# Performance work log

Hardware: AMD Instinct MI355X
Metric: run time of the kernel (lower is better)

The kernel has to match this reference:

```python
import jax, jax.numpy as jnp
import numpy as np

N, E, F, U, H = 10000, 160000, 128, 128, 8
BN_EPS = 1e-3  # keras BatchNormalization default


def _batch_norm(x, gamma, beta):
    # GraphBatchNormalization in training mode: stats over the flat node/edge axis
    mean = jnp.mean(x, axis=0, keepdims=True)
    var = jnp.var(x, axis=0, keepdims=True)
    return (x - mean) * jax.lax.rsqrt(var + BN_EPS) * gamma + beta


def setup_inputs() -> dict:
    key = jax.random.key(0)
    k = jax.random.split(key, 12)
    s = 0.1  # weight init scale
    return {
        "node_attributes": jax.random.normal(k[0], (N, F), jnp.float32),
        "edge_attributes": jax.random.normal(k[1], (E, F), jnp.float32),
        "edge_indices": jax.random.randint(k[2], (E, 2), 0, N, jnp.int32),
        "W_edge": jax.random.normal(k[3], (3 * F, U), jnp.float32) * s,
        "b_edge": jnp.zeros((U,), jnp.float32),
        "gamma_e": jnp.ones((U,), jnp.float32),
        "beta_e": jnp.zeros((U,), jnp.float32),
        "W_node": jax.random.normal(k[4], (F, U), jnp.float32) * s,
        "b_node": jnp.zeros((U,), jnp.float32),
        "gamma_n": jnp.ones((U,), jnp.float32),
        "beta_n": jnp.zeros((U,), jnp.float32),
        "W_att": jax.random.normal(k[5], (H, F, U), jnp.float32) * s,
        "b_att": jnp.zeros((H, U), jnp.float32),
        "a_att": jax.random.normal(k[6], (H, 3 * U), jnp.float32) * s,
        "gru_kernel": jax.random.normal(k[7], (U, 3 * U), jnp.float32) * s,
        "gru_rkernel": jax.random.normal(k[8], (U, 3 * U), jnp.float32) * s,
        "gru_bias": jnp.zeros((2, 3 * U), jnp.float32),
    }


def reference(node_attributes, edge_attributes, edge_indices, W_edge, b_edge,
              gamma_e, beta_e, W_node, b_node, gamma_n, beta_n,
              W_att, b_att, a_att, gru_kernel, gru_rkernel, gru_bias):
    dst = edge_indices[:, 0]  # receiving (ingoing) node per edge
    src = edge_indices[:, 1]  # sending (outgoing) node per edge

    # gather -> concat -> edge MLP -> graph batch norm
    edge_in = node_attributes[src]   # GatherNodesOutgoing
    edge_out = node_attributes[dst]  # GatherNodesIngoing
    edge_concat = jnp.concatenate([edge_in, edge_out, edge_attributes], axis=-1)  # [E, 3F]
    edge_updated = jax.nn.relu(edge_concat @ W_edge + b_edge)
    edge_updated = _batch_norm(edge_updated, gamma_e, beta_e)  # [E, U]

    # multi-head GAT attention over edges, aggregated to receiving node
    z = jnp.einsum('nf,hfu->hnu', node_attributes, W_att) + b_att[:, None, :]  # [H,N,U]
    a_src, a_dst, a_edge = jnp.split(a_att, 3, axis=-1)  # each [H,U]
    s_src = jnp.einsum('hnu,hu->hn', z, a_src)[:, src]           # [H,E]
    s_dst = jnp.einsum('hnu,hu->hn', z, a_dst)[:, dst]           # [H,E]
    s_edge = jnp.einsum('eu,hu->he', edge_updated, a_edge)       # [H,E]
    logits = jax.nn.leaky_relu(s_src + s_dst + s_edge, 0.2)

    seg_max = jax.vmap(lambda l: jax.ops.segment_max(l, dst, num_segments=N))(logits)  # [H,N]
    ex = jnp.exp(logits - seg_max[:, dst])
    den = jax.vmap(lambda e: jax.ops.segment_sum(e, dst, num_segments=N))(ex)          # [H,N]
    alpha = ex / den[:, dst]                                                            # [H,E]

    msgs = alpha[:, :, None] * z[:, src]  # [H,E,U]
    agg = jax.vmap(lambda m: jax.ops.segment_sum(m, dst, num_segments=N))(msgs)  # [H,N,U]
    node_attended = jax.nn.relu(jnp.mean(agg, axis=0))  # [N,U]

    # node MLP + graph batch norm
    node_updated = jax.nn.relu(node_attributes @ W_node + b_node)
    node_updated = _batch_norm(node_updated, gamma_n, beta_n)  # [N,U]

    # GRU update (keras GRUCell, reset_after=True): input=node_attended, state=node_updated
    mx = node_attended @ gru_kernel + gru_bias[0]
    mi = node_updated @ gru_rkernel + gru_bias[1]
    xz, xr, xh = jnp.split(mx, 3, axis=-1)
    rz, rr, rh = jnp.split(mi, 3, axis=-1)
    zg = jax.nn.sigmoid(xz + rz)
    rg = jax.nn.sigmoid(xr + rr)
    hh = jnp.tanh(xh + rg * rh)
    node_final = zg * node_updated + (1.0 - zg) * hh

    return node_final, edge_updated
```

## Files before the change

### kernel.cpp

```cpp
#include <hip/hip_runtime.h>
#include <hip/hip_bf16.h>

#define NN 10000
#define EE 160000
#define FF 128
#define UU 128
#define HH 8
#define BN_EPS 1e-3f

typedef __attribute__((ext_vector_type(8))) short bf16x8;
typedef __attribute__((ext_vector_type(8))) unsigned short u16x8;
typedef __attribute__((ext_vector_type(4))) unsigned short u16x4;
typedef __attribute__((ext_vector_type(4))) unsigned int u32x4;
typedef __attribute__((ext_vector_type(4))) float f32x4;
typedef __attribute__((ext_vector_type(2))) float f32x2;

static __device__ __forceinline__ unsigned short f2bf(float f) {
    unsigned u = __float_as_uint(f);
    u += 0x7fffu + ((u >> 16) & 1u);
    return (unsigned short)(u >> 16);
}
static __device__ __forceinline__ float bf2f(unsigned short b) {
    return __uint_as_float((unsigned)b << 16);
}

__global__ void k_prep(const float* __restrict__ node, unsigned short* __restrict__ node_bf,
                       const float* __restrict__ We, unsigned short* __restrict__ WtE,
                       const float* __restrict__ Wn, unsigned short* __restrict__ WnT,
                       const float* __restrict__ Watt, unsigned short* __restrict__ WtA,
                       const float* __restrict__ Wk, const float* __restrict__ Wr,
                       unsigned short* __restrict__ WcT) {
    int b = blockIdx.x, t = threadIdx.x;
    if (b < 1250) {
        int i = b * 256 + t;
        float4 v = reinterpret_cast<const float4*>(node)[i];
        ushort4 o;
        o.x = f2bf(v.x); o.y = f2bf(v.y); o.z = f2bf(v.z); o.w = f2bf(v.w);
        reinterpret_cast<ushort4*>(node_bf)[i] = o;
    } else if (b < 1442) {
        int i = (b - 1250) * 256 + t;
        int s = i >> 14, rem = i & 16383, u = rem >> 7, k = rem & 127;
        WtE[i] = f2bf(We[(s * 128 + k) * 128 + u]);
    } else if (b < 1506) {
        int i = (b - 1442) * 256 + t;
        int k = i >> 7, u = i & 127;
        WnT[u * 128 + k] = f2bf(Wn[i]);
    } else if (b < 2018) {
        int i = (b - 1506) * 256 + t;
        int h = i >> 14, rem = i & 16383, f = rem >> 7, u = rem & 127;
        WtA[h * 16384 + u * 128 + f] = f2bf(Watt[i]);
    } else {
        int i = (b - 2018) * 256 + t;
        int c = i >> 8, k = i & 255;
        float v;
        if (c < 256)       v = (k < 128) ? Wk[k * 384 + c] : Wr[(k - 128) * 384 + c];
        else if (c < 384)  v = (k < 128) ? Wk[k * 384 + c] : 0.f;
        else               v = (k < 128) ? 0.f : Wr[(k - 128) * 384 + (c - 128)];
        WcT[c * 256 + k] = f2bf(v);
    }
}

__global__ void k_hist(const int* __restrict__ eidx, int* __restrict__ cnt, int E) {
    int e = blockIdx.x * 256 + threadIdx.x;
    if (e < E) atomicAdd(&cnt[eidx[2 * e]], 1);
}

__global__ void k_scan(const int* __restrict__ cnt, int* __restrict__ off,
                       int* __restrict__ cursor, int N) {
    __shared__ int wpre[16];
    __shared__ int runsh;
    int t = threadIdx.x, lane = t & 63, wv = t >> 6;
    if (t == 0) { off[0] = 0; runsh = 0; }
    __syncthreads();
    for (int base = 0; base < N; base += 1024) {
        int x = (base + t < N) ? cnt[base + t] : 0;
        int s = x;
#pragma unroll
        for (int o = 1; o < 64; o <<= 1) {
            int v = __shfl_up(s, o, 64);
            if (lane >= o) s += v;
        }
        if (lane == 63) wpre[wv] = s;
        __syncthreads();
        if (t == 0) {
            int acc = runsh;
#pragma unroll
            for (int i = 0; i < 16; ++i) { int tmp = wpre[i]; wpre[i] = acc; acc += tmp; }
            runsh = acc;
        }
        __syncthreads();
        int inc = s + wpre[wv];
        if (base + t < N) {
            off[base + t + 1] = inc;
            cursor[base + t] = inc - x;
        }
        __syncthreads();
    }
}

__global__ void k_scatter(const int* __restrict__ eidx, int* __restrict__ cursor,
                          int* __restrict__ elist, int E) {
    int e = blockIdx.x * 256 + threadIdx.x;
    if (e < E) {
        int d = eidx[2 * e];
        int p = atomicAdd(&cursor[d], 1);
        elist[p] = e;
    }
}

__global__ void __launch_bounds__(256) k_z8(
        const unsigned short* __restrict__ node_bf, const unsigned short* __restrict__ WtA,
        const float* __restrict__ batt, const float* __restrict__ aatt,
        unsigned char* __restrict__ zt8, float* __restrict__ s_src, float* __restrict__ s_dst) {
    __shared__ unsigned short lds[16 * 1032];
    int n0 = blockIdx.x * 16;
    int t = threadIdx.x;
    {
        int r = t >> 4, c = t & 15;
        *reinterpret_cast<uint4*>(&lds[r * 136 + c * 8]) =
            *reinterpret_cast<const uint4*>(node_bf + (size_t)(n0 + r) * 128 + c * 8);
    }
    __syncthreads();

    int wid = t >> 6, lane = t & 63;
    int lr = lane & 15, lg = lane >> 4;

    f32x4 acc[2][8];
#pragma unroll
    for (int hh = 0; hh < 2; ++hh)
#pragma unroll
        for (int nt = 0; nt < 8; ++nt) acc[hh][nt] = (f32x4){0.f, 0.f, 0.f, 0.f};

#pragma unroll
    for (int ks = 0; ks < 4; ++ks) {
        int kb = ks * 32 + lg * 8;
        bf16x8 a = *reinterpret_cast<const bf16x8*>(&lds[lr * 136 + kb]);
#pragma unroll
        for (int hh = 0; hh < 2; ++hh) {
            const unsigned short* Wh = WtA + (size_t)(wid * 2 + hh) * 16384;
#pragma unroll
            for (int nt = 0; nt < 8; ++nt) {
                bf16x8 b = *reinterpret_cast<const bf16x8*>(Wh + (size_t)(nt * 16 + lr) * 128 + kb);
                acc[hh][nt] = __builtin_amdgcn_mfma_f32_16x16x32_bf16(a, b, acc[hh][nt], 0, 0, 0);
            }
        }
    }

    __syncthreads();
    int head0 = wid * 2, head1 = wid * 2 + 1;
    float ps[2][4], pd[2][4];
#pragma unroll
    for (int hh = 0; hh < 2; ++hh)
#pragma unroll
        for (int r = 0; r < 4; ++r) { ps[hh][r] = 0.f; pd[hh][r] = 0.f; }

#pragma unroll
    for (int nt = 0; nt < 8; ++nt) {
        int col = nt * 16 + lr;
        float b0 = batt[head0 * 128 + col], b1 = batt[head1 * 128 + col];
        float as0 = aatt[head0 * 384 + col], ad0 = aatt[head0 * 384 + 128 + col];
        float as1 = aatt[head1 * 384 + col], ad1 = aatt[head1 * 384 + 128 + col];
#pragma unroll
        for (int r = 0; r < 4; ++r) {
            int row = lg * 4 + r;
            float z0 = acc[0][nt][r] + b0;
            float z1 = acc[1][nt][r] + b1;
            unsigned pk = __builtin_amdgcn_cvt_pk_fp8_f32(z0, z1, 0, false);
            lds[row * 520 + col * 4 + wid] = (unsigned short)(pk & 0xffffu);
            ps[0][r] = fmaf(z0, as0, ps[0][r]);
            pd[0][r] = fmaf(z0, ad0, pd[0][r]);
            ps[1][r] = fmaf(z1, as1, ps[1][r]);
            pd[1][r] = fmaf(z1, ad1, pd[1][r]);
        }
    }
#pragma unroll
    for (int o = 1; o < 16; o <<= 1) {
#pragma unroll
        for (int hh = 0; hh < 2; ++hh)
#pragma unroll
            for (int r = 0; r < 4; ++r) {
                ps[hh][r] += __shfl_xor(ps[hh][r], o, 64);
                pd[hh][r] += __shfl_xor(pd[hh][r], o, 64);
            }
    }
    if (lr == 0) {
#pragma unroll
        for (int hh = 0; hh < 2; ++hh) {
            int head = wid * 2 + hh;
#pragma unroll
            for (int r = 0; r < 4; ++r) {
                int n = n0 + lg * 4 + r;
                s_src[n * 8 + head] = ps[hh][r];
                s_dst[n * 8 + head] = pd[hh][r];
            }
        }
    }
    __syncthreads();
    unsigned short* zt8u = reinterpret_cast<unsigned short*>(zt8);
    for (int q = t; q < 16 * 64; q += 256) {
        int row = q >> 6, c = q & 63;
        *reinterpret_cast<uint4*>(&zt8u[(size_t)(n0 + row) * 512 + c * 8]) =
            *reinterpret_cast<const uint4*>(&lds[row * 520 + c * 8]);
    }
}

__global__ void k_lsum(const float* __restrict__ s_src, const float* __restrict__ s_edge,
                       const int* __restrict__ elist, const int* __restrict__ eidx,
                       float* __restrict__ ls, int* __restrict__ srcl) {
    int p = blockIdx.x * 256 + threadIdx.x;
    if (p >= EE) return;
    int e = elist[p];
    int src = eidx[2 * e + 1];
    srcl[p] = src;
    float4 a0 = *reinterpret_cast<const float4*>(s_src + (size_t)src * 8);
    float4 a1 = *reinterpret_cast<const float4*>(s_src + (size_t)src * 8 + 4);
    float4 b0 = *reinterpret_cast<const float4*>(s_edge + (size_t)e * 8);
    float4 b1 = *reinterpret_cast<const float4*>(s_edge + (size_t)e * 8 + 4);
    float4 o0, o1;
    o0.x = a0.x + b0.x; o0.y = a0.y + b0.y; o0.z = a0.z + b0.z; o0.w = a0.w + b0.w;
    o1.x = a1.x + b1.x; o1.y = a1.y + b1.y; o1.z = a1.z + b1.z; o1.w = a1.w + b1.w;
    *reinterpret_cast<float4*>(ls + (size_t)p * 8) = o0;
    *reinterpret_cast<float4*>(ls + (size_t)p * 8 + 4) = o1;
}

__global__ void __launch_bounds__(256) k_p12_mfma(
        const unsigned short* __restrict__ node_bf, const unsigned short* __restrict__ WtE,
        unsigned short* __restrict__ p12, int N) {
    __shared__ unsigned short ash[64][136];
    int n0 = blockIdx.x * 64;
    int s = blockIdx.y;
    int t = threadIdx.x;
    for (int q = t; q < 64 * 16; q += 256) {
        int r = q >> 4, c = q & 15;
        int n = n0 + r; if (n >= N) n = N - 1;
        *reinterpret_cast<uint4*>(&ash[r][c * 8]) =
            *reinterpret_cast<const uint4*>(node_bf + (size_t)n * 128 + c * 8);
    }
    __syncthreads();

    int wid = t >> 6, lane = t & 63;
    int wm = wid >> 1, wn = wid & 1;
    int lr = lane & 15, lg = lane >> 4;

    f32x4 acc[2][4];
#pragma unroll
    for (int m = 0; m < 2; ++m)
#pragma unroll
        for (int n = 0; n < 4; ++n) acc[m][n] = (f32x4){0.f, 0.f, 0.f, 0.f};

    const unsigned short* Wh = WtE + (size_t)s * 16384;
#pragma unroll
    for (int ks = 0; ks < 4; ++ks) {
        int kb = ks * 32 + lg * 8;
        bf16x8 a0 = *reinterpret_cast<const bf16x8*>(&ash[wm * 32 + lr][kb]);
        bf16x8 a1 = *reinterpret_cast<const bf16x8*>(&ash[wm * 32 + 16 + lr][kb]);
        bf16x8 b[4];
#pragma unroll
        for (int n = 0; n < 4; ++n)
            b[n] = *reinterpret_cast<const bf16x8*>(Wh + (size_t)(wn * 64 + n * 16 + lr) * 128 + kb);
#pragma unroll
        for (int n = 0; n < 4; ++n) {
            acc[0][n] = __builtin_amdgcn_mfma_f32_16x16x32_bf16(a0, b[n], acc[0][n], 0, 0, 0);
            acc[1][n] = __builtin_amdgcn_mfma_f32_16x16x32_bf16(a1, b[n], acc[1][n], 0, 0, 0);
        }
    }

    __syncthreads();
    unsigned short* ot = &ash[0][0];
#pragma unroll
    for (int n = 0; n < 4; ++n) {
        int col = wn * 64 + n * 16 + lr;
#pragma unroll
        for (int m = 0; m < 2; ++m) {
            int rowb = wm * 32 + m * 16 + lg * 4;
#pragma unroll
            for (int r = 0; r < 4; ++r)
                ot[(rowb + r) * 136 + col] = f2bf(acc[m][n][r]);
        }
    }
    __syncthreads();
    for (int q = t; q < 64 * 16; q += 256) {
        int r = q >> 4, c = q & 15;
        int row = n0 + r;
        if (row < N)
            *reinterpret_cast<uint4*>(&p12[(size_t)row * 256 + s * 128 + c * 8]) =
                *reinterpret_cast<const uint4*>(&ot[r * 136 + c * 8]);
    }
}

__global__ void __launch_bounds__(256) k_pe_comb(
        const float* __restrict__ eattr, const unsigned short* __restrict__ WtE,
        const float* __restrict__ be, const unsigned short* __restrict__ p12,
        const int* __restrict__ eidx, unsigned short* __restrict__ ebuf,
        float* __restrict__ part) {
    __shared__ unsigned short ash[64][136];
    __shared__ unsigned short pcomb[64][136];
    __shared__ int sd[128];
    __shared__ float sbuf[4][64], qbuf[4][64];
    int e0 = blockIdx.x * 64;
    int t = threadIdx.x;
    if (t < 128) sd[t] = eidx[e0 * 2 + t];
    __syncthreads();
    for (int q = t; q < 64 * 32; q += 256) {
        int r = q >> 5, c = q & 31;
        f32x4 v = __builtin_nontemporal_load(
            reinterpret_cast<const f32x4*>(eattr + (size_t)(e0 + r) * 128 + c * 4));
        ushort4 o;
        o.x = f2bf(v.x); o.y = f2bf(v.y); o.z = f2bf(v.z); o.w = f2bf(v.w);
        *reinterpret_cast<ushort4*>(&ash[r][c * 4]) = o;
    }
    for (int q = t; q < 64 * 16; q += 256) {
        int r = q >> 4, c = q & 15;
        int dst = sd[r * 2], src = sd[r * 2 + 1];
        u16x8 a = *reinterpret_cast<const u16x8*>(p12 + (size_t)src * 256 + c * 8);
        u16x8 b = *reinterpret_cast<const u16x8*>(p12 + (size_t)dst * 256 + 128 + c * 8);
        u16x8 o;
#pragma unroll
        for (int j = 0; j < 8; ++j) o[j] = f2bf(bf2f(a[j]) + bf2f(b[j]));
        *reinterpret_cast<u16x8*>(&pcomb[r][c * 8]) = o;
    }
    __syncthreads();

    int wid = t >> 6, lane = t & 63;
    int wm = wid >> 1, wn = wid & 1;
    int lr = lane & 15, lg = lane >> 4;

    f32x4 acc[2][4];
#pragma unroll
    for (int m = 0; m < 2; ++m)
#pragma unroll
        for (int n = 0; n < 4; ++n) acc[m][n] = (f32x4){0.f, 0.f, 0.f, 0.f};

    const unsigned short* Wh = WtE + (size_t)2 * 16384;
#pragma unroll
    for (int ks = 0; ks < 4; ++ks) {
        int kb = ks * 32 + lg * 8;
        bf16x8 a0 = *reinterpret_cast<const bf16x8*>(&ash[wm * 32 + lr][kb]);
        bf16x8 a1 = *reinterpret_cast<const bf16x8*>(&ash[wm * 32 + 16 + lr][kb]);
        bf16x8 b[4];
#pragma unroll
        for (int n = 0; n < 4; ++n)
            b[n] = *reinterpret_cast<const bf16x8*>(Wh + (size_t)(wn * 64 + n * 16 + lr) * 128 + kb);
#pragma unroll
        for (int n = 0; n < 4; ++n) {
            acc[0][n] = __builtin_amdgcn_mfma_f32_16x16x32_bf16(a0, b[n], acc[0][n], 0, 0, 0);
            acc[1][n] = __builtin_amdgcn_mfma_f32_16x16x32_bf16(a1, b[n], acc[1][n], 0, 0, 0);
        }
    }

    __syncthreads();
    unsigned short* ot = &ash[0][0];
    float s[4] = {0.f, 0.f, 0.f, 0.f}, q[4] = {0.f, 0.f, 0.f, 0.f};
#pragma unroll
    for (int n = 0; n < 4; ++n) {
        int col = wn * 64 + n * 16 + lr;
        float bias = be[col];
#pragma unroll
        for (int m = 0; m < 2; ++m) {
            int rowb = wm * 32 + m * 16 + lg * 4;
#pragma unroll
            for (int r = 0; r < 4; ++r) {
                int row = rowb + r;
                float v = acc[m][n][r] + bias + bf2f(pcomb[row][col]);
                v = v > 0.f ? v : 0.f;
                ot[row * 136 + col] = f2bf(v);
                s[n] += v;
                q[n] += v * v;
            }
        }
    }
#pragma unroll
    for (int n = 0; n < 4; ++n) {
        s[n] += __shfl_xor(s[n], 16, 64);
        s[n] += __shfl_xor(s[n], 32, 64);
        q[n] += __shfl_xor(q[n], 16, 64);
        q[n] += __shfl_xor(q[n], 32, 64);
    }
    if (lane < 16) {
#pragma unroll
        for (int n = 0; n < 4; ++n) {
            sbuf[wid][n * 16 + lane] = s[n];
            qbuf[wid][n * 16 + lane] = q[n];
        }
    }
    __syncthreads();
    for (int q2 = t; q2 < 64 * 16; q2 += 256) {
        int r = q2 >> 4, c = q2 & 15;
        *reinterpret_cast<uint4*>(&ebuf[(size_t)(e0 + r) * 128 + c * 8]) =
            *reinterpret_cast<const uint4*>(&ot[r * 136 + c * 8]);
    }
    if (t < 128) {
        int half = t >> 6, c = t & 63;
        part[(size_t)blockIdx.x * 256 + t] = sbuf[half][c] + sbuf[2 + half][c];
        part[(size_t)blockIdx.x * 256 + 128 + t] = qbuf[half][c] + qbuf[2 + half][c];
    }
}

__global__ void __launch_bounds__(256) k_node_mlp_mfma(
        const unsigned short* __restrict__ node_bf, const unsigned short* __restrict__ WnT,
        const float* __restrict__ bn, unsigned short* __restrict__ nupd_bf,
        float* __restrict__ part, int N) {
    __shared__ unsigned short ash[64][136];
    __shared__ float sbuf[4][64], qbuf[4][64];
    int n0 = blockIdx.x * 64;
    int t = threadIdx.x;
    for (int q = t; q < 64 * 16; q += 256) {
        int r = q >> 4, c = q & 15;
        int n = n0 + r; if (n >= N) n = N - 1;
        *reinterpret_cast<uint4*>(&ash[r][c * 8]) =
            *reinterpret_cast<const uint4*>(node_bf + (size_t)n * 128 + c * 8);
    }
    __syncthreads();

    int wid = t >> 6, lane = t & 63;
    int wm = wid >> 1, wn = wid & 1;
    int lr = lane & 15, lg = lane >> 4;

    f32x4 acc[2][4];
#pragma unroll
    for (int m = 0; m < 2; ++m)
#pragma unroll
        for (int n = 0; n < 4; ++n) acc[m][n] = (f32x4){0.f, 0.f, 0.f, 0.f};

#pragma unroll
    for (int ks = 0; ks < 4; ++ks) {
        int kb = ks * 32 + lg * 8;
        bf16x8 a0 = *reinterpret_cast<const bf16x8*>(&ash[wm * 32 + lr][kb]);
        bf16x8 a1 = *reinterpret_cast<const bf16x8*>(&ash[wm * 32 + 16 + lr][kb]);
        bf16x8 b[4];
#pragma unroll
        for (int n = 0; n < 4; ++n)
            b[n] = *reinterpret_cast<const bf16x8*>(WnT + (size_t)(wn * 64 + n * 16 + lr) * 128 + kb);
#pragma unroll
        for (int n = 0; n < 4; ++n) {
            acc[0][n] = __builtin_amdgcn_mfma_f32_16x16x32_bf16(a0, b[n], acc[0][n], 0, 0, 0);
            acc[1][n] = __builtin_amdgcn_mfma_f32_16x16x32_bf16(a1, b[n], acc[1][n], 0, 0, 0);
        }
    }

    __syncthreads();
    unsigned short* ot = &ash[0][0];
    float s[4] = {0.f, 0.f, 0.f, 0.f}, q[4] = {0.f, 0.f, 0.f, 0.f};
#pragma unroll
    for (int n = 0; n < 4; ++n) {
        int col = wn * 64 + n * 16 + lr;
        float bias = bn[col];
#pragma unroll
        for (int m = 0; m < 2; ++m) {
            int rowb = wm * 32 + m * 16 + lg * 4;
#pragma unroll
            for (int r = 0; r < 4; ++r) {
                int row = n0 + rowb + r;
                float v = acc[m][n][r] + bias;
                v = v > 0.f ? v : 0.f;
                ot[(rowb + r) * 136 + col] = f2bf(v);
                if (row < N) { s[n] += v; q[n] += v * v; }
            }
        }
    }
#pragma unroll
    for (int n = 0; n < 4; ++n) {
        s[n] += __shfl_xor(s[n], 16, 64);
        s[n] += __shfl_xor(s[n], 32, 64);
        q[n] += __shfl_xor(q[n], 16, 64);
        q[n] += __shfl_xor(q[n], 32, 64);
    }
    if (lane < 16) {
#pragma unroll
        for (int n = 0; n < 4; ++n) {
            sbuf[wid][n * 16 + lane] = s[n];
            qbuf[wid][n * 16 + lane] = q[n];
        }
    }
    __syncthreads();
    for (int q2 = t; q2 < 64 * 16; q2 += 256) {
        int r = q2 >> 4, c = q2 & 15;
        int row = n0 + r;
        if (row < N)
            *reinterpret_cast<uint4*>(&nupd_bf[(size_t)row * 128 + c * 8]) =
                *reinterpret_cast<const uint4*>(&ot[r * 136 + c * 8]);
    }
    if (t < 128) {
        int half = t >> 6, c = t & 63;
        part[(size_t)blockIdx.x * 256 + t] = sbuf[half][c] + sbuf[2 + half][c];
        part[(size_t)blockIdx.x * 256 + 128 + t] = qbuf[half][c] + qbuf[2 + half][c];
    }
}

__global__ void k_bn_fin(const float* __restrict__ part, int nblk, float invcnt,
                         const float* __restrict__ g, const float* __restrict__ b,
                         float* __restrict__ scale, float* __restrict__ shift) {
    int u = blockIdx.x;
    int t = threadIdx.x;
    float s = 0.f, q = 0.f;
    for (int i = t; i < nblk; i += 256) {
        s += part[(size_t)i * 256 + u];
        q += part[(size_t)i * 256 + 128 + u];
    }
    __shared__ float ls[4], lq[4];
    for (int o = 32; o > 0; o >>= 1) {
        s += __shfl_down(s, o, 64);
        q += __shfl_down(q, o, 64);
    }
    int lane = t & 63, w = t >> 6;
    if (lane == 0) { ls[w] = s; lq[w] = q; }
    __syncthreads();
    if (t == 0) {
        float S = ls[0] + ls[1] + ls[2] + ls[3];
        float Q = lq[0] + lq[1] + lq[2] + lq[3];
        float mean = S * invcnt;
        float var = Q * invcnt - mean * mean;
        float inv = rsqrtf(var + BN_EPS);
        float sc = g[u] * inv;
        scale[u] = sc;
        shift[u] = b[u] - mean * sc;
    }
}

__global__ void __launch_bounds__(256) k_edge_final(
        const unsigned short* __restrict__ ebuf, const float* __restrict__ scale,
        const float* __restrict__ shift, const float* __restrict__ aatt,
        float* __restrict__ eout, float* __restrict__ s_edge) {
    int t = threadIdx.x;
    int w = t >> 6, lane = t & 63;
    int q = lane & 31, half = lane >> 5;
    int e = blockIdx.x * 8 + w * 2 + half;

    float4 sc = *reinterpret_cast<const float4*>(scale + q * 4);
    float4 sh = *reinterpret_cast<const float4*>(shift + q * 4);
    float4 a4[8];
#pragma unroll
    for (int h = 0; h < 8; ++h)
        a4[h] = *reinterpret_cast<const float4*>(aatt + h * 384 + 256 + q * 4);

    ushort4 xb = *reinterpret_cast<const ushort4*>(ebuf + (size_t)e * 128 + q * 4);
    float4 x;
    x.x = bf2f(xb.x) * sc.x + sh.x;
    x.y = bf2f(xb.y) * sc.y + sh.y;
    x.z = bf2f(xb.z) * sc.z + sh.z;
    x.w = bf2f(xb.w) * sc.w + sh.w;
    *reinterpret_cast<float4*>(eout + (size_t)e * 128 + q * 4) = x;

    float v[8];
#pragma unroll
    for (int h = 0; h < 8; ++h)
        v[h] = x.x * a4[h].x + x.y * a4[h].y + x.z * a4[h].z + x.w * a4[h].w;
#pragma unroll
    for (int o = 1; o < 32; o <<= 1) {
#pragma unroll
        for (int h = 0; h < 8; ++h) v[h] += __shfl_xor(v[h], o, 64);
    }
    if (q == 0) {
#pragma unroll
        for (int h = 0; h < 8; ++h) s_edge[e * 8 + h] = v[h];
    }
}

__global__ void __launch_bounds__(256) k_agg(
        const unsigned char* __restrict__ zt8, const float* __restrict__ ls,
        const int* __restrict__ srcl, const float* __restrict__ s_dst,
        const int* __restrict__ off, unsigned short* __restrict__ cat) {
    int wv = threadIdx.x >> 6, lane = threadIdx.x & 63;
    int n = blockIdx.x * 4 + wv;
    __shared__ float wbuf[4][64][8];
    __shared__ int snbuf[4][64];

    int beg = off[n], end = off[n + 1];
    int deg = end - beg;
    if (deg == 0) {
        cat[(size_t)n * 256 + lane] = 0;
        cat[(size_t)n * 256 + 64 + lane] = 0;
        return;
    }

    float sdh[8];
#pragma unroll
    for (int h = 0; h < 8; ++h) sdh[h] = s_dst[n * 8 + h];

    float den[8], a0v[8], a1v[8];
#pragma unroll
    for (int h = 0; h < 8; ++h) { den[h] = 0.f; a0v[h] = 0.f; a1v[h] = 0.f; }

    for (int c0 = 0; c0 < deg; c0 += 64) {
        int cn = min(64, deg - c0);
        if (lane < cn) {
            int p = beg + c0 + lane;
            snbuf[wv][lane] = srcl[p];
            float4 l0 = *reinterpret_cast<const float4*>(ls + (size_t)p * 8);
            float4 l1 = *reinterpret_cast<const float4*>(ls + (size_t)p * 8 + 4);
            float lg[8] = {l0.x, l0.y, l0.z, l0.w, l1.x, l1.y, l1.z, l1.w};
#pragma unroll
            for (int h = 0; h < 8; ++h) {
                float x = lg[h] + sdh[h];
                x = x >= 0.f ? x : 0.2f * x;
                wbuf[wv][lane][h] = __expf(x);
            }
        }
        for (int i = 0; i < cn; ++i) {
            int sn_i = snbuf[wv][i];
            const unsigned char* zr = zt8 + (size_t)sn_i * 1024 + (size_t)lane * 8;
            uint2 zv0 = *reinterpret_cast<const uint2*>(zr);
            uint2 zv1 = *reinterpret_cast<const uint2*>(zr + 512);
            float4 w0 = *reinterpret_cast<const float4*>(&wbuf[wv][i][0]);
            float4 w1 = *reinterpret_cast<const float4*>(&wbuf[wv][i][4]);
            f32x2 q01 = __builtin_amdgcn_cvt_pk_f32_fp8(zv0.x, false);
            f32x2 q23 = __builtin_amdgcn_cvt_pk_f32_fp8(zv0.x, true);
            f32x2 q45 = __builtin_amdgcn_cvt_pk_f32_fp8(zv0.y, false);
            f32x2 q67 = __builtin_amdgcn_cvt_pk_f32_fp8(zv0.y, true);
            f32x2 r01 = __builtin_amdgcn_cvt_pk_f32_fp8(zv1.x, false);
            f32x2 r23 = __builtin_amdgcn_cvt_pk_f32_fp8(zv1.x, true);
            f32x2 r45 = __builtin_amdgcn_cvt_pk_f32_fp8(zv1.y, false);
            f32x2 r67 = __builtin_amdgcn_cvt_pk_f32_fp8(zv1.y, true);
            den[0] += w0.x; a0v[0] = fmaf(w0.x, q01.x, a0v[0]); a1v[0] = fmaf(w0.x, r01.x, a1v[0]);
            den[1] += w0.y; a0v[1] = fmaf(w0.y, q01.y, a0v[1]); a1v[1] = fmaf(w0.y, r01.y, a1v[1]);
            den[2] += w0.z; a0v[2] = fmaf(w0.z, q23.x, a0v[2]); a1v[2] = fmaf(w0.z, r23.x, a1v[2]);
            den[3] += w0.w; a0v[3] = fmaf(w0.w, q23.y, a0v[3]); a1v[3] = fmaf(w0.w, r23.y, a1v[3]);
            den[4] += w1.x; a0v[4] = fmaf(w1.x, q45.x, a0v[4]); a1v[4] = fmaf(w1.x, r45.x, a1v[4]);
            den[5] += w1.y; a0v[5] = fmaf(w1.y, q45.y, a0v[5]); a1v[5] = fmaf(w1.y, r45.y, a1v[5]);
            den[6] += w1.z; a0v[6] = fmaf(w1.z, q67.x, a0v[6]); a1v[6] = fmaf(w1.z, r67.x, a1v[6]);
            den[7] += w1.w; a0v[7] = fmaf(w1.w, q67.y, a0v[7]); a1v[7] = fmaf(w1.w, r67.y, a1v[7]);
        }
    }
    float r0 = 0.f, r1 = 0.f;
#pragma unroll
    for (int h = 0; h < 8; ++h) {
        float inv = 1.f / den[h];
        r0 = fmaf(a0v[h], inv, r0);
        r1 = fmaf(a1v[h], inv, r1);
    }
    cat[(size_t)n * 256 + lane] = f2bf(fmaxf(r0 * 0.125f, 0.f));
    cat[(size_t)n * 256 + 64 + lane] = f2bf(fmaxf(r1 * 0.125f, 0.f));
}

__global__ void k_gru_pre(const unsigned short* __restrict__ nupd_bf, const float* __restrict__ scale,
                          const float* __restrict__ shift, unsigned short* __restrict__ cat,
                          float* __restrict__ ush) {
    int i = blockIdx.x * 256 + threadIdx.x;
    if (i >= NN * 32) return;
    int n = i >> 5, j4 = (i & 31) * 4;
    ushort4 ub_in = *reinterpret_cast<const ushort4*>(nupd_bf + (size_t)n * 128 + j4);
    float4 sc = *reinterpret_cast<const float4*>(scale + j4);
    float4 sh = *reinterpret_cast<const float4*>(shift + j4);
    float4 uv;
    uv.x = bf2f(ub_in.x) * sc.x + sh.x;
    uv.y = bf2f(ub_in.y) * sc.y + sh.y;
    uv.z = bf2f(ub_in.z) * sc.z + sh.z;
    uv.w = bf2f(ub_in.w) * sc.w + sh.w;
    ushort4 ub;
    ub.x = f2bf(uv.x); ub.y = f2bf(uv.y); ub.z = f2bf(uv.z); ub.w = f2bf(uv.w);
    *reinterpret_cast<ushort4*>(cat + (size_t)n * 256 + 128 + j4) = ub;
    *reinterpret_cast<float4*>(ush + (size_t)n * 128 + j4) = uv;
}

__global__ void __launch_bounds__(256) k_gru_mm(
        const unsigned short* __restrict__ cat, const unsigned short* __restrict__ WcT,
        float* __restrict__ S, int N) {
    __shared__ unsigned short ash[64][264];
    int n0 = blockIdx.x * 64;
    int g = blockIdx.y;
    int t = threadIdx.x;
    for (int q = t; q < 64 * 32; q += 256) {
        int r = q >> 5, c = q & 31;
        int n = n0 + r; if (n >= N) n = N - 1;
        *reinterpret_cast<uint4*>(&ash[r][c * 8]) =
            *reinterpret_cast<const uint4*>(cat + (size_t)n * 256 + c * 8);
    }
    __syncthreads();

    int wid = t >> 6, lane = t & 63;
    int wm = wid >> 1, wn = wid & 1;
    int lr = lane & 15, lg = lane >> 4;

    f32x4 acc[2][4];
#pragma unroll
    for (int m = 0; m < 2; ++m)
#pragma unroll
        for (int n = 0; n < 4; ++n) acc[m][n] = (f32x4){0.f, 0.f, 0.f, 0.f};

    const unsigned short* Wg = WcT + (size_t)g * 128 * 256;
#pragma unroll
    for (int ks = 0; ks < 8; ++ks) {
        int kb = ks * 32 + lg * 8;
        bf16x8 a0 = *reinterpret_cast<const bf16x8*>(&ash[wm * 32 + lr][kb]);
        bf16x8 a1 = *reinterpret_cast<const bf16x8*>(&ash[wm * 32 + 16 + lr][kb]);
        bf16x8 b[4];
#pragma unroll
        for (int n = 0; n < 4; ++n)
            b[n] = *reinterpret_cast<const bf16x8*>(Wg + (size_t)(wn * 64 + n * 16 + lr) * 256 + kb);
#pragma unroll
        for (int n = 0; n < 4; ++n) {
            acc[0][n] = __builtin_amdgcn_mfma_f32_16x16x32_bf16(a0, b[n], acc[0][n], 0, 0, 0);
            acc[1][n] = __builtin_amdgcn_mfma_f32_16x16x32_bf16(a1, b[n], acc[1][n], 0, 0, 0);
        }
    }

    __syncthreads();
    float* otf = reinterpret_cast<float*>(&ash[0][0]);
#pragma unroll
    for (int n = 0; n < 4; ++n) {
        int col = wn * 64 + n * 16 + lr;
#pragma unroll
        for (int m = 0; m < 2; ++m) {
            int rowb = wm * 32 + m * 16 + lg * 4;
#pragma unroll
            for (int r = 0; r < 4; ++r)
                otf[(rowb + r) * 132 + col] = acc[m][n][r];
        }
    }
    __syncthreads();
    for (int q = t; q < 64 * 32; q += 256) {
        int r = q >> 5, c = q & 31;
        int row = n0 + r;
        if (row < N)
            *reinterpret_cast<float4*>(&S[(size_t)row * 512 + g * 128 + c * 4]) =
                *reinterpret_cast<const float4*>(&otf[r * 132 + c * 4]);
    }
}

__global__ void __launch_bounds__(256) k_gru_gates(
        const float* __restrict__ S, const float* __restrict__ ush,
        const float* __restrict__ gbias, float* __restrict__ outp) {
    int t = threadIdx.x;
    int n = blockIdx.x * 2 + (t >> 7);
    int u = t & 127;
    const float* b0 = gbias;
    const float* b1 = gbias + 384;
    float s0 = S[(size_t)n * 512 + u];
    float s1 = S[(size_t)n * 512 + 128 + u];
    float xh = S[(size_t)n * 512 + 256 + u];
    float rh = S[(size_t)n * 512 + 384 + u];
    float zg = 1.f / (1.f + __expf(-(s0 + b0[u] + b1[u])));
    float rg = 1.f / (1.f + __expf(-(s1 + b0[128 + u] + b1[128 + u])));
    float hh = tanhf(xh + b0[256 + u] + rg * (rh + b1[256 + u]));
    float uv = ush[(size_t)n * 128 + u];
    outp[(size_t)n * 128 + u] = zg * uv + (1.f - zg) * hh;
}

extern "C" void kernel_launch(void* const* d_in, const int* in_sizes, int n_in,
                              void* d_out, int out_size, void* d_ws, size_t ws_size,
                              hipStream_t stream) {
    const float* node    = (const float*)d_in[0];
    const float* eattr   = (const float*)d_in[1];
    const int*   eidx    = (const int*)d_in[2];
    const float* We      = (const float*)d_in[3];
    const float* be      = (const float*)d_in[4];
    const float* gamma_e = (const float*)d_in[5];
    const float* beta_e  = (const float*)d_in[6];
    const float* Wn      = (const float*)d_in[7];
    const float* bnb     = (const float*)d_in[8];
    const float* gamma_n = (const float*)d_in[9];
    const float* beta_n  = (const float*)d_in[10];
    const float* Watt    = (const float*)d_in[11];
    const float* batt    = (const float*)d_in[12];
    const float* aatt    = (const float*)d_in[13];
    const float* Wk      = (const float*)d_in[14];
    const float* Wr      = (const float*)d_in[15];
    const float* gbias   = (const float*)d_in[16];

    float* out_node = (float*)d_out;
    float* out_edge = out_node + (size_t)NN * UU;

    char* wp = (char*)d_ws;
    auto alloc = [&](size_t bytes) {
        void* p = (void*)wp;
        wp += (bytes + 255) / 256 * 256;
        return p;
    };
    unsigned char* zt8   = (unsigned char*)alloc((size_t)NN * 1024);
    unsigned short* ebuf = (unsigned short*)alloc((size_t)EE * 128 * 2);
    float* s_src   = (float*)alloc((size_t)NN * 8 * 4);
    float* s_dst   = (float*)alloc((size_t)NN * 8 * 4);
    float* s_edge  = (float*)alloc((size_t)EE * 8 * 4);
    float* lsbuf   = (float*)alloc((size_t)EE * 8 * 4);
    int*   srcl    = (int*)alloc((size_t)EE * 4);
    float* part_e  = (float*)alloc((size_t)2500 * 256 * 4);
    float* part_n  = (float*)alloc((size_t)157 * 256 * 4);
    float* scale_e = (float*)alloc(512);
    float* shift_e = (float*)alloc(512);
    float* scale_n = (float*)alloc(512);
    float* shift_n = (float*)alloc(512);
    unsigned short* nupd_bf = (unsigned short*)alloc((size_t)NN * 128 * 2);
    float* ush     = (float*)alloc((size_t)NN * 128 * 4);
    float* Sbuf    = (float*)alloc((size_t)NN * 512 * 4);
    int*   cnt     = (int*)alloc((size_t)NN * 4);
    int*   offs    = (int*)alloc((size_t)(NN + 1) * 4);
    int*   cursor  = (int*)alloc((size_t)NN * 4);
    int*   elist   = (int*)alloc((size_t)EE * 4);
    unsigned short* node_bf = (unsigned short*)alloc((size_t)NN * 128 * 2);
    unsigned short* WtE     = (unsigned short*)alloc((size_t)3 * 128 * 128 * 2);
    unsigned short* WtA     = (unsigned short*)alloc((size_t)8 * 128 * 128 * 2);
    unsigned short* WnT     = (unsigned short*)alloc((size_t)128 * 128 * 2);
    unsigned short* WcT     = (unsigned short*)alloc((size_t)512 * 256 * 2);
    unsigned short* cat     = (unsigned short*)alloc((size_t)NN * 256 * 2);
    unsigned short* p12     = (unsigned short*)alloc((size_t)NN * 256 * 2);

    hipMemsetAsync(cnt, 0, (size_t)NN * 4, stream);
    k_hist<<<(EE + 255) / 256, 256, 0, stream>>>(eidx, cnt, EE);
    k_scan<<<1, 1024, 0, stream>>>(cnt, offs, cursor, NN);
    k_scatter<<<(EE + 255) / 256, 256, 0, stream>>>(eidx, cursor, elist, EE);

    k_prep<<<2530, 256, 0, stream>>>(node, node_bf, We, WtE, Wn, WnT, Watt, WtA, Wk, Wr, WcT);

    k_p12_mfma<<<dim3((NN + 63) / 64, 2), 256, 0, stream>>>(node_bf, WtE, p12, NN);
    k_pe_comb<<<EE / 64, 256, 0, stream>>>(eattr, WtE, be, p12, eidx, ebuf, part_e);
    k_bn_fin<<<128, 256, 0, stream>>>(part_e, EE / 64, 1.f / (float)EE,
                                      gamma_e, beta_e, scale_e, shift_e);
    k_edge_final<<<EE / 8, 256, 0, stream>>>(ebuf, scale_e, shift_e, aatt, out_edge, s_edge);

    k_z8<<<NN / 16, 256, 0, stream>>>(node_bf, WtA, batt, aatt, zt8, s_src, s_dst);
    k_lsum<<<(EE + 255) / 256, 256, 0, stream>>>(s_src, s_edge, elist, eidx, lsbuf, srcl);
    k_agg<<<NN / 4, 256, 0, stream>>>(zt8, lsbuf, srcl, s_dst, offs, cat);

    k_node_mlp_mfma<<<(NN + 63) / 64, 256, 0, stream>>>(node_bf, WnT, bnb, nupd_bf, part_n, NN);
    k_bn_fin<<<128, 256, 0, stream>>>(part_n, (NN + 63) / 64, 1.f / (float)NN,
                                      gamma_n, beta_n, scale_n, shift_n);

    k_gru_pre<<<(NN * 32 + 255) / 256, 256, 0, stream>>>(nupd_bf, scale_n, shift_n, cat, ush);
    k_gru_mm<<<dim3((NN + 63) / 64, 4), 256, 0, stream>>>(cat, WcT, Sbuf, NN);
    k_gru_gates<<<NN / 2, 256, 0, stream>>>(Sbuf, ush, gbias, out_node);
}
```

Before: 245.8 us.

## Fuse edge-logit sum into edge_final and merge the two BN finalize kernels

k_scatter now also records each edge's CSR position. k_edge_final uses it to add s_src and write the dst-sorted logit sums and src list directly, which removes the separate k_lsum pass and the s_edge buffer. The two batch-norm finalize launches are merged into one 256-block kernel, and k_z8 and the node MLP are moved earlier so their outputs are ready. This saves two launches and one E×8 round trip through memory, at the cost of scattered writes to ls and srcl from k_edge_final.

```diff
diff --git a/kernel.cpp b/kernel.cpp
--- a/kernel.cpp
+++ b/kernel.cpp
@@ -99,12 +99,13 @@
 }
 
 __global__ void k_scatter(const int* __restrict__ eidx, int* __restrict__ cursor,
-                          int* __restrict__ elist, int E) {
+                          int* __restrict__ elist, int* __restrict__ pos, int E) {
     int e = blockIdx.x * 256 + threadIdx.x;
     if (e < E) {
         int d = eidx[2 * e];
         int p = atomicAdd(&cursor[d], 1);
         elist[p] = e;
+        pos[e] = p;
     }
 }
 
@@ -202,25 +203,6 @@
         *reinterpret_cast<uint4*>(&zt8u[(size_t)(n0 + row) * 512 + c * 8]) =
             *reinterpret_cast<const uint4*>(&lds[row * 520 + c * 8]);
     }
-}
-
-__global__ void k_lsum(const float* __restrict__ s_src, const float* __restrict__ s_edge,
-                       const int* __restrict__ elist, const int* __restrict__ eidx,
-                       float* __restrict__ ls, int* __restrict__ srcl) {
-    int p = blockIdx.x * 256 + threadIdx.x;
-    if (p >= EE) return;
-    int e = elist[p];
-    int src = eidx[2 * e + 1];
-    srcl[p] = src;
-    float4 a0 = *reinterpret_cast<const float4*>(s_src + (size_t)src * 8);
-    float4 a1 = *reinterpret_cast<const float4*>(s_src + (size_t)src * 8 + 4);
-    float4 b0 = *reinterpret_cast<const float4*>(s_edge + (size_t)e * 8);
-    float4 b1 = *reinterpret_cast<const float4*>(s_edge + (size_t)e * 8 + 4);
-    float4 o0, o1;
-    o0.x = a0.x + b0.x; o0.y = a0.y + b0.y; o0.z = a0.z + b0.z; o0.w = a0.w + b0.w;
-    o1.x = a1.x + b1.x; o1.y = a1.y + b1.y; o1.z = a1.z + b1.z; o1.w = a1.w + b1.w;
-    *reinterpret_cast<float4*>(ls + (size_t)p * 8) = o0;
-    *reinterpret_cast<float4*>(ls + (size_t)p * 8 + 4) = o1;
 }
 
 __global__ void __launch_bounds__(256) k_p12_mfma(
@@ -487,10 +469,22 @@
     }
 }
 
-__global__ void k_bn_fin(const float* __restrict__ part, int nblk, float invcnt,
-                         const float* __restrict__ g, const float* __restrict__ b,
-                         float* __restrict__ scale, float* __restrict__ shift) {
-    int u = blockIdx.x;
+__global__ void k_bn_fin2(const float* __restrict__ part_e, int nblk_e, float invcnt_e,
+                          const float* __restrict__ g_e, const float* __restrict__ b_e,
+                          float* __restrict__ scale_e, float* __restrict__ shift_e,
+                          const float* __restrict__ part_n, int nblk_n, float invcnt_n,
+                          const float* __restrict__ g_n, const float* __restrict__ b_n,
+                          float* __restrict__ scale_n, float* __restrict__ shift_n) {
+    bool is_edge = blockIdx.x < 128;
+    int u = is_edge ? blockIdx.x : blockIdx.x - 128;
+    const float* part = is_edge ? part_e : part_n;
+    int nblk = is_edge ? nblk_e : nblk_n;
+    float invcnt = is_edge ? invcnt_e : invcnt_n;
+    const float* g = is_edge ? g_e : g_n;
+    const float* b = is_edge ? b_e : b_n;
+    float* scale = is_edge ? scale_e : scale_n;
+    float* shift = is_edge ? shift_e : shift_n;
+
     int t = threadIdx.x;
     float s = 0.f, q = 0.f;
     for (int i = t; i < nblk; i += 256) {
@@ -520,7 +514,9 @@
 __global__ void __launch_bounds__(256) k_edge_final(
         const unsigned short* __restrict__ ebuf, const float* __restrict__ scale,
         const float* __restrict__ shift, const float* __restrict__ aatt,
-        float* __restrict__ eout, float* __restrict__ s_edge) {
+        const int* __restrict__ eidx, const int* __restrict__ pos,
+        const float* __restrict__ s_src,
+        float* __restrict__ eout, float* __restrict__ ls, int* __restrict__ srcl) {
     int t = threadIdx.x;
     int w = t >> 6, lane = t & 63;
     int q = lane & 31, half = lane >> 5;
@@ -551,8 +547,16 @@
         for (int h = 0; h < 8; ++h) v[h] += __shfl_xor(v[h], o, 64);
     }
     if (q == 0) {
-#pragma unroll
-        for (int h = 0; h < 8; ++h) s_edge[e * 8 + h] = v[h];
+        int src = eidx[2 * e + 1];
+        int p = pos[e];
+        srcl[p] = src;
+        float4 a0 = *reinterpret_cast<const float4*>(s_src + (size_t)src * 8);
+        float4 a1 = *reinterpret_cast<const float4*>(s_src + (size_t)src * 8 + 4);
+        float4 o0, o1;
+        o0.x = v[0] + a0.x; o0.y = v[1] + a0.y; o0.z = v[2] + a0.z; o0.w = v[3] + a0.w;
+        o1.x = v[4] + a1.x; o1.y = v[5] + a1.y; o1.z = v[6] + a1.z; o1.w = v[7] + a1.w;
+        *reinterpret_cast<float4*>(ls + (size_t)p * 8) = o0;
+        *reinterpret_cast<float4*>(ls + (size_t)p * 8 + 4) = o1;
     }
 }
 
@@ -770,7 +774,6 @@
     unsigned short* ebuf = (unsigned short*)alloc((size_t)EE * 128 * 2);
     float* s_src   = (float*)alloc((size_t)NN * 8 * 4);
     float* s_dst   = (float*)alloc((size_t)NN * 8 * 4);
-    float* s_edge  = (float*)alloc((size_t)EE * 8 * 4);
     float* lsbuf   = (float*)alloc((size_t)EE * 8 * 4);
     int*   srcl    = (int*)alloc((size_t)EE * 4);
     float* part_e  = (float*)alloc((size_t)2500 * 256 * 4);
@@ -786,6 +789,7 @@
     int*   offs    = (int*)alloc((size_t)(NN + 1) * 4);
     int*   cursor  = (int*)alloc((size_t)NN * 4);
     int*   elist   = (int*)alloc((size_t)EE * 4);
+    int*   pos     = (int*)alloc((size_t)EE * 4);
     unsigned short* node_bf = (unsigned short*)alloc((size_t)NN * 128 * 2);
     unsigned short* WtE     = (unsigned short*)alloc((size_t)3 * 128 * 128 * 2);
     unsigned short* WtA     = (unsigned short*)alloc((size_t)8 * 128 * 128 * 2);
@@ -797,24 +801,21 @@
     hipMemsetAsync(cnt, 0, (size_t)NN * 4, stream);
     k_hist<<<(EE + 255) / 256, 256, 0, stream>>>(eidx, cnt, EE);
     k_scan<<<1, 1024, 0, stream>>>(cnt, offs, cursor, NN);
-    k_scatter<<<(EE + 255) / 256, 256, 0, stream>>>(eidx, cursor, elist, EE);
+    k_scatter<<<(EE + 255) / 256, 256, 0, stream>>>(eidx, cursor, elist, pos, EE);
 
     k_prep<<<2530, 256, 0, stream>>>(node, node_bf, We, WtE, Wn, WnT, Watt, WtA, Wk, Wr, WcT);
+
+    k_z8<<<NN / 16, 256, 0, stream>>>(node_bf, WtA, batt, aatt, zt8, s_src, s_dst);
+    k_node_mlp_mfma<<<(NN + 63) / 64, 256, 0, stream>>>(node_bf, WnT, bnb, nupd_bf, part_n, NN);
 
     k_p12_mfma<<<dim3((NN + 63) / 64, 2), 256, 0, stream>>>(node_bf, WtE, p12, NN);
     k_pe_comb<<<EE / 64, 256, 0, stream>>>(eattr, WtE, be, p12, eidx, ebuf, part_e);
-    k_bn_fin<<<128, 256, 0, stream>>>(part_e, EE / 64, 1.f / (float)EE,
-                                      gamma_e, beta_e, scale_e, shift_e);
-    k_edge_final<<<EE / 8, 256, 0, stream>>>(ebuf, scale_e, shift_e, aatt, out_edge, s_edge);
-
-    k_z8<<<NN / 16, 256, 0, stream>>>(node_bf, WtA, batt, aatt, zt8, s_src, s_dst);
-    k_lsum<<<(EE + 255) / 256, 256, 0, stream>>>(s_src, s_edge, elist, eidx, lsbuf, srcl);
+    k_bn_fin2<<<256, 256, 0, stream>>>(part_e, EE / 64, 1.f / (float)EE, gamma_e, beta_e, scale_e, shift_e,
+                                       part_n, (NN + 63) / 64, 1.f / (float)NN, gamma_n, beta_n, scale_n, shift_n);
+    k_edge_final<<<EE / 8, 256, 0, stream>>>(ebuf, scale_e, shift_e, aatt, eidx, pos, s_src,
+                                             out_edge, lsbuf, srcl);
+
     k_agg<<<NN / 4, 256, 0, stream>>>(zt8, lsbuf, srcl, s_dst, offs, cat);
-
-    k_node_mlp_mfma<<<(NN + 63) / 64, 256, 0, stream>>>(node_bf, WnT, bnb, nupd_bf, part_n, NN);
-    k_bn_fin<<<128, 256, 0, stream>>>(part_n, (NN + 63) / 64, 1.f / (float)NN,
-                                      gamma_n, beta_n, scale_n, shift_n);
-
     k_gru_pre<<<(NN * 32 + 255) / 256, 256, 0, stream>>>(nupd_bf, scale_n, shift_n, cat, ush);
     k_gru_mm<<<dim3((NN + 63) / 64, 4), 256, 0, stream>>>(cat, WcT, Sbuf, NN);
     k_gru_gates<<<NN / 2, 256, 0, stream>>>(Sbuf, ush, gbias, out_node);
```

Result: faster. 240.1 us (median of 2 runs) (-2.3%).
